# Performance work log

Hardware: AMD Instinct MI355X
Metric: run time of the kernel (lower is better)

## Reference

```python
import jax, jax.numpy as jnp
import numpy as np

N = 262144  # total points
D = 256     # embedding dim
S = 8       # number of subbatches
L = 64      # instance labels per subbatch (label id range)
DELTA_V = 0.5
DELTA_D = 1.5


def setup_inputs() -> dict:
    key = jax.random.key(0)
    k1, k2, k3 = jax.random.split(key, 3)
    outputs = jax.random.normal(k1, (N, D), dtype=jnp.float32)
    labels = jax.random.randint(k2, (N,), 0, L, dtype=jnp.int32)
    subbatch_indices = jax.random.randint(k3, (N,), 0, S, dtype=jnp.int32)
    return {"outputs": outputs, "labels": labels, "subbatch_indices": subbatch_indices}


def reference(outputs, labels, subbatch_indices):
    n = outputs.shape[0]
    # normalize embeddings (L2 norm per point, matching torch.linalg.norm axis=1)
    x = outputs / (jnp.linalg.norm(outputs, axis=1) + 1e-8)[:, None]

    # combined segment id: (subbatch, label) -> subbatch*L + label
    seg = subbatch_indices * L + labels  # [N]
    num_seg = S * L

    ones = jnp.ones((n,), dtype=x.dtype)
    counts = jax.ops.segment_sum(ones, seg, num_segments=num_seg)        # [S*L] Nm per (sb,label)
    sums = jax.ops.segment_sum(x, seg, num_segments=num_seg)             # [S*L, D]
    mus = sums / jnp.maximum(counts, 1.0)[:, None]                        # centroids
    present = counts > 0                                                  # [S*L]
    M = jnp.sum(present.reshape(S, L).astype(x.dtype), axis=1)            # [S] unique labels per subbatch

    # ---- pull term: sum_m sum_{i in m} relu(||mu_m - x_i||_1 - dv)^2 / (M*Nm) ----
    mu_pt = mus[seg]                                                      # [N, D]
    d1 = jnp.sum(jnp.abs(mu_pt - x), axis=1)                              # [N] L1 dist to own centroid
    pull_pt = jax.nn.relu(d1 - DELTA_V) ** 2                              # weights are all 1.0
    denom = M[subbatch_indices] * counts[seg]                             # [N] M_sb * Nm
    L_pull = jax.ops.segment_sum(pull_pt / denom, subbatch_indices, num_segments=S)  # [S]

    # ---- push term: pairwise centroid L1 distances within each subbatch ----
    mus_s = mus.reshape(S, L, D)
    pres = present.reshape(S, L)
    dist = jnp.sum(jnp.abs(mus_s[:, :, None, :] - mus_s[:, None, :, :]), axis=-1)  # [S,L,L]
    pairmask = pres[:, :, None] & pres[:, None, :]
    pairmask = pairmask & (~jnp.eye(L, dtype=bool))[None]
    push = jnp.sum(jnp.where(pairmask, jax.nn.relu(2.0 * DELTA_D - dist) ** 2, 0.0), axis=(1, 2))
    L_push = push / jnp.maximum(M * (M - 1.0), 1.0)                        # [S]

    # only subbatches with M > 1 contribute; divide by B = total number of points
    valid = M > 1.0
    loss = jnp.sum(jnp.where(valid, L_pull + L_push, 0.0)) / n
    return loss
```

## Files before the change

### kernel.cpp

```cpp
#include <hip/hip_runtime.h>

#define DIM 256
#define NSB 8
#define NLBL 64
#define NSEG (NSB * NLBL)
#define NBH 128
#define CAP 576
#define SMEM_BYTES (CAP * 256 + DIM * 4 + 16 * 4)

__global__ void k_hist(const int* __restrict__ labels, const int* __restrict__ sbidx,
                       int* __restrict__ blockBins, int n) {
    __shared__ int bins[NSEG];
    for (int i = threadIdx.x; i < NSEG; i += 256) bins[i] = 0;
    __syncthreads();
    int t4 = blockIdx.x * 256 + threadIdx.x;
    int stride4 = gridDim.x * 256;
    for (int q = t4; q * 4 < n; q += stride4) {
        int4 lb = reinterpret_cast<const int4*>(labels)[q];
        int4 sb = reinterpret_cast<const int4*>(sbidx)[q];
        atomicAdd(&bins[sb.x * NLBL + lb.x], 1);
        atomicAdd(&bins[sb.y * NLBL + lb.y], 1);
        atomicAdd(&bins[sb.z * NLBL + lb.z], 1);
        atomicAdd(&bins[sb.w * NLBL + lb.w], 1);
    }
    __syncthreads();
    for (int i = threadIdx.x; i < NSEG; i += 256)
        blockBins[blockIdx.x * NSEG + i] = bins[i];
}

__global__ void k_scan(const int* __restrict__ blockBins, int* __restrict__ counts,
                       int* __restrict__ offsets, int* __restrict__ cursors,
                       float* __restrict__ Mvals, float* __restrict__ invcnt,
                       float* __restrict__ Lpull, float* __restrict__ pushv,
                       int* __restrict__ ticket) {
    __shared__ int cnt[NSEG];
    int t = threadIdx.x;
    int sum = 0;
    #pragma unroll 4
    for (int b = 0; b < NBH; b++) sum += blockBins[b * NSEG + t];
    cnt[t] = sum;
    counts[t] = sum;
    invcnt[t] = 1.0f / fmaxf((float)sum, 1.0f);
    if (t < NSB) { Lpull[t] = 0.f; pushv[t] = 0.f; }
    if (t == 0) ticket[0] = 0;
    __syncthreads();
    if (t < 64) {
        int lane = t;
        int carry = 0;
        for (int c = 0; c < NSB; c++) {
            int idx = c * 64 + lane;
            int v = cnt[idx];
            int incl = v;
            #pragma unroll
            for (int m = 1; m < 64; m <<= 1) {
                int t2 = __shfl_up(incl, m, 64);
                if (lane >= m) incl += t2;
            }
            int excl = carry + incl - v;
            offsets[idx] = excl;
            cursors[idx] = excl;
            carry += __shfl(incl, 63, 64);
            unsigned long long b = __ballot(v > 0);
            if (lane == 0) Mvals[c] = (float)__popcll(b);
        }
    }
}

__global__ void k_scatter(const int* __restrict__ labels, const int* __restrict__ sbidx,
                          int* __restrict__ cursors, int* __restrict__ sorted, int n) {
    int t = blockIdx.x * blockDim.x + threadIdx.x;
    int stride = gridDim.x * blockDim.x;
    for (int q = t; q * 4 < n; q += stride) {
        int4 lb = reinterpret_cast<const int4*>(labels)[q];
        int4 sb = reinterpret_cast<const int4*>(sbidx)[q];
        int p = q * 4;
        sorted[atomicAdd(&cursors[sb.x * NLBL + lb.x], 1)] = p;
        sorted[atomicAdd(&cursors[sb.y * NLBL + lb.y], 1)] = p + 1;
        sorted[atomicAdd(&cursors[sb.z * NLBL + lb.z], 1)] = p + 2;
        sorted[atomicAdd(&cursors[sb.w * NLBL + lb.w], 1)] = p + 3;
    }
}

__device__ inline unsigned packq(float x, float y, float z, float w, float s) {
    int q0 = (int)rintf(x * s); q0 = max(-127, min(127, q0));
    int q1 = (int)rintf(y * s); q1 = max(-127, min(127, q1));
    int q2 = (int)rintf(z * s); q2 = max(-127, min(127, q2));
    int q3 = (int)rintf(w * s); q3 = max(-127, min(127, q3));
    return (unsigned)(q0 & 255) | ((unsigned)(q1 & 255) << 8) |
           ((unsigned)(q2 & 255) << 16) | ((unsigned)(q3 & 255) << 24);
}

__global__ __launch_bounds__(1024) void k_seg(
    const float* __restrict__ outp, const int* __restrict__ sorted,
    const int* __restrict__ offsets, const int* __restrict__ counts,
    const float* __restrict__ invcnt, float* __restrict__ mus,
    float* __restrict__ Lpull) {
    extern __shared__ unsigned char smem[];
    unsigned* xrows = (unsigned*)smem;
    float* muA  = (float*)(smem + CAP * 256);
    float* wsum = (float*)(smem + CAP * 256 + DIM * 4);

    int seg = blockIdx.x;
    int base = offsets[seg], cnt = counts[seg];
    int tid = threadIdx.x, lane = tid & 63, wv = tid >> 6;
    float ic = invcnt[seg];
    if (tid < DIM) muA[tid] = 0.f;
    __syncthreads();
    if (cnt == 0) {
        if (tid < DIM) mus[(size_t)seg * DIM + tid] = 0.f;
        return;
    }

    float4 acc = {0.f, 0.f, 0.f, 0.f};
    int r = wv * 4;
    int p0 = (r + 0 < cnt) ? sorted[base + r + 0] : -1;
    int p1 = (r + 1 < cnt) ? sorted[base + r + 1] : -1;
    int p2 = (r + 2 < cnt) ? sorted[base + r + 2] : -1;
    int p3 = (r + 3 < cnt) ? sorted[base + r + 3] : -1;
    for (; r < cnt; r += 64) {
        int nr = r + 64;
        int q0 = (nr + 0 < cnt) ? sorted[base + nr + 0] : -1;
        int q1 = (nr + 1 < cnt) ? sorted[base + nr + 1] : -1;
        int q2 = (nr + 2 < cnt) ? sorted[base + nr + 2] : -1;
        int q3 = (nr + 3 < cnt) ? sorted[base + nr + 3] : -1;
        float4 v0 = {0.f,0.f,0.f,0.f}, v1 = {0.f,0.f,0.f,0.f};
        float4 v2 = {0.f,0.f,0.f,0.f}, v3 = {0.f,0.f,0.f,0.f};
        v0 = *reinterpret_cast<const float4*>(outp + (size_t)p0 * DIM + lane * 4);
        if (p1 >= 0) v1 = *reinterpret_cast<const float4*>(outp + (size_t)p1 * DIM + lane * 4);
        if (p2 >= 0) v2 = *reinterpret_cast<const float4*>(outp + (size_t)p2 * DIM + lane * 4);
        if (p3 >= 0) v3 = *reinterpret_cast<const float4*>(outp + (size_t)p3 * DIM + lane * 4);
        float s0 = v0.x*v0.x + v0.y*v0.y + v0.z*v0.z + v0.w*v0.w;
        float s1 = v1.x*v1.x + v1.y*v1.y + v1.z*v1.z + v1.w*v1.w;
        float s2 = v2.x*v2.x + v2.y*v2.y + v2.z*v2.z + v2.w*v2.w;
        float s3 = v3.x*v3.x + v3.y*v3.y + v3.z*v3.z + v3.w*v3.w;
        #pragma unroll
        for (int m = 32; m >= 1; m >>= 1) {
            s0 += __shfl_xor(s0, m, 64);
            s1 += __shfl_xor(s1, m, 64);
            s2 += __shfl_xor(s2, m, 64);
            s3 += __shfl_xor(s3, m, 64);
        }
        float r0 = 1.0f / (sqrtf(s0) + 1e-8f);
        float r1 = 1.0f / (sqrtf(s1) + 1e-8f);
        float r2 = 1.0f / (sqrtf(s2) + 1e-8f);
        float r3 = 1.0f / (sqrtf(s3) + 1e-8f);
        if (r + 0 < CAP)            xrows[(r + 0) * 64 + lane] = packq(v0.x, v0.y, v0.z, v0.w, r0 * 256.f);
        if (p1 >= 0 && r + 1 < CAP) xrows[(r + 1) * 64 + lane] = packq(v1.x, v1.y, v1.z, v1.w, r1 * 256.f);
        if (p2 >= 0 && r + 2 < CAP) xrows[(r + 2) * 64 + lane] = packq(v2.x, v2.y, v2.z, v2.w, r2 * 256.f);
        if (p3 >= 0 && r + 3 < CAP) xrows[(r + 3) * 64 + lane] = packq(v3.x, v3.y, v3.z, v3.w, r3 * 256.f);
        acc.x += v0.x*r0 + v1.x*r1 + v2.x*r2 + v3.x*r3;
        acc.y += v0.y*r0 + v1.y*r1 + v2.y*r2 + v3.y*r3;
        acc.z += v0.z*r0 + v1.z*r1 + v2.z*r2 + v3.z*r3;
        acc.w += v0.w*r0 + v1.w*r1 + v2.w*r2 + v3.w*r3;
        p0 = q0; p1 = q1; p2 = q2; p3 = q3;
    }
    atomicAdd(&muA[lane * 4 + 0], acc.x);
    atomicAdd(&muA[lane * 4 + 1], acc.y);
    atomicAdd(&muA[lane * 4 + 2], acc.z);
    atomicAdd(&muA[lane * 4 + 3], acc.w);
    __syncthreads();
    if (tid < DIM) {
        float mu = muA[tid] * ic;
        muA[tid] = mu;
        mus[(size_t)seg * DIM + tid] = mu;
    }
    __syncthreads();

    float4 mu4 = *reinterpret_cast<const float4*>(muA + lane * 4);
    float4 mu256 = {mu4.x * 256.f, mu4.y * 256.f, mu4.z * 256.f, mu4.w * 256.f};
    float psum = 0.f;
    int m1 = min(cnt, CAP);
    for (int rr = wv * 4; rr < m1; rr += 64) {
        bool b1 = rr + 1 < m1, b2 = rr + 2 < m1, b3 = rr + 3 < m1;
        unsigned w0 = xrows[(rr + 0) * 64 + lane];
        unsigned w1 = b1 ? xrows[(rr + 1) * 64 + lane] : 0u;
        unsigned w2 = b2 ? xrows[(rr + 2) * 64 + lane] : 0u;
        unsigned w3 = b3 ? xrows[(rr + 3) * 64 + lane] : 0u;
        float d0 = fabsf(mu256.x - (float)((int)(w0 << 24) >> 24))
                 + fabsf(mu256.y - (float)((int)(w0 << 16) >> 24))
                 + fabsf(mu256.z - (float)((int)(w0 <<  8) >> 24))
                 + fabsf(mu256.w - (float)((int)w0 >> 24));
        float d1 = fabsf(mu256.x - (float)((int)(w1 << 24) >> 24))
                 + fabsf(mu256.y - (float)((int)(w1 << 16) >> 24))
                 + fabsf(mu256.z - (float)((int)(w1 <<  8) >> 24))
                 + fabsf(mu256.w - (float)((int)w1 >> 24));
        float d2 = fabsf(mu256.x - (float)((int)(w2 << 24) >> 24))
                 + fabsf(mu256.y - (float)((int)(w2 << 16) >> 24))
                 + fabsf(mu256.z - (float)((int)(w2 <<  8) >> 24))
                 + fabsf(mu256.w - (float)((int)w2 >> 24));
        float d3 = fabsf(mu256.x - (float)((int)(w3 << 24) >> 24))
                 + fabsf(mu256.y - (float)((int)(w3 << 16) >> 24))
                 + fabsf(mu256.z - (float)((int)(w3 <<  8) >> 24))
                 + fabsf(mu256.w - (float)((int)w3 >> 24));
        #pragma unroll
        for (int m = 32; m >= 1; m >>= 1) {
            d0 += __shfl_xor(d0, m, 64);
            d1 += __shfl_xor(d1, m, 64);
            d2 += __shfl_xor(d2, m, 64);
            d3 += __shfl_xor(d3, m, 64);
        }
        float t0 = fmaxf(d0 * 0.00390625f - 0.5f, 0.f);
        psum += t0 * t0;
        if (b1) { float t = fmaxf(d1 * 0.00390625f - 0.5f, 0.f); psum += t * t; }
        if (b2) { float t = fmaxf(d2 * 0.00390625f - 0.5f, 0.f); psum += t * t; }
        if (b3) { float t = fmaxf(d3 * 0.00390625f - 0.5f, 0.f); psum += t * t; }
    }
    for (int rr = CAP + wv; rr < cnt; rr += 16) {
        int p = sorted[base + rr];
        float4 v = *reinterpret_cast<const float4*>(outp + (size_t)p * DIM + lane * 4);
        float ss = v.x*v.x + v.y*v.y + v.z*v.z + v.w*v.w;
        #pragma unroll
        for (int m = 32; m >= 1; m >>= 1) ss += __shfl_xor(ss, m, 64);
        float rn = 1.0f / (sqrtf(ss) + 1e-8f);
        float d = fabsf(mu4.x - v.x*rn) + fabsf(mu4.y - v.y*rn)
                + fabsf(mu4.z - v.z*rn) + fabsf(mu4.w - v.w*rn);
        #pragma unroll
        for (int m = 32; m >= 1; m >>= 1) d += __shfl_xor(d, m, 64);
        float t = fmaxf(d - 0.5f, 0.f);
        psum += t * t;
    }
    if (lane == 0) wsum[wv] = psum;
    __syncthreads();
    if (tid == 0) {
        float tot = 0.f;
        #pragma unroll
        for (int w = 0; w < 16; w++) tot += wsum[w];
        atomicAdd(&Lpull[seg >> 6], tot * ic);
    }
}

__global__ void k_final(const float* __restrict__ mus, const int* __restrict__ counts,
                        float* __restrict__ pushv, float* __restrict__ Lpull,
                        const float* __restrict__ Mvals, int* __restrict__ ticket,
                        float* __restrict__ outv, int n) {
    __shared__ float lds[NLBL][DIM + 1];
    __shared__ float wsum[4];
    __shared__ int lastFlag;
    int s = blockIdx.x >> 4;
    int chunk = blockIdx.x & 15;
    for (int i = threadIdx.x; i < NLBL * DIM; i += 256) {
        int r = i >> 8, d = i & 255;
        lds[r][d] = mus[(size_t)(s * NLBL + r) * DIM + d];
    }
    __syncthreads();
    int pair = chunk * 256 + threadIdx.x;
    int l1 = pair >> 6, l2 = pair & 63;
    float dist = 0.0f;
    #pragma unroll 8
    for (int d = 0; d < DIM; d++) dist += fabsf(lds[l1][d] - lds[l2][d]);
    float v = fmaxf(3.0f - dist, 0.0f);
    v = v * v;
    bool ok = (l1 != l2) && (counts[s * NLBL + l1] > 0) && (counts[s * NLBL + l2] > 0);
    v = ok ? v : 0.0f;
    #pragma unroll
    for (int m = 32; m >= 1; m >>= 1) v += __shfl_xor(v, m, 64);
    if ((threadIdx.x & 63) == 0) wsum[threadIdx.x >> 6] = v;
    __syncthreads();
    if (threadIdx.x == 0) {
        atomicAdd(&pushv[s], wsum[0] + wsum[1] + wsum[2] + wsum[3]);
        __threadfence();
        int t = atomicAdd(ticket, 1);
        lastFlag = (t == (int)gridDim.x - 1) ? 1 : 0;
    }
    __syncthreads();
    if (lastFlag && threadIdx.x == 0) {
        float loss = 0.0f;
        for (int q = 0; q < NSB; q++) {
            float M = Mvals[q];
            float pv = atomicAdd(&pushv[q], 0.0f);
            float lpv = atomicAdd(&Lpull[q], 0.0f);
            if (M > 1.0f)
                loss += lpv / M + pv / fmaxf(M * (M - 1.0f), 1.0f);
        }
        outv[0] = loss / (float)n;
    }
}

extern "C" void kernel_launch(void* const* d_in, const int* in_sizes, int n_in,
                              void* d_out, int out_size, void* d_ws, size_t ws_size,
                              hipStream_t stream) {
    const float* outp = (const float*)d_in[0];
    const int* labels = (const int*)d_in[1];
    const int* sbidx = (const int*)d_in[2];
    float* outv = (float*)d_out;
    int n = in_sizes[1];

    float* mus = (float*)d_ws;
    int* sorted = (int*)(mus + (size_t)NSEG * DIM);
    int* blockBins = sorted + n;
    int* counts = blockBins + NBH * NSEG;
    int* offsets = counts + NSEG;
    int* cursors = offsets + NSEG;
    int* ticket = cursors + NSEG;
    float* invcnt = (float*)(ticket + 1);
    float* Mvals = invcnt + NSEG;
    float* Lpull = Mvals + NSB;
    float* pushv = Lpull + NSB;

    hipFuncSetAttribute(reinterpret_cast<const void*>(k_seg),
                        hipFuncAttributeMaxDynamicSharedMemorySize, SMEM_BYTES);

    k_hist<<<NBH, 256, 0, stream>>>(labels, sbidx, blockBins, n);
    k_scan<<<1, 512, 0, stream>>>(blockBins, counts, offsets, cursors, Mvals, invcnt,
                                  Lpull, pushv, ticket);
    k_scatter<<<256, 256, 0, stream>>>(labels, sbidx, cursors, sorted, n);
    k_seg<<<NSEG, 1024, SMEM_BYTES, stream>>>(outp, sorted, offsets, counts, invcnt,
                                              mus, Lpull);
    k_final<<<NSB * 16, 256, 0, stream>>>(mus, counts, pushv, Lpull, Mvals,
                                          ticket, outv, n);
}
```

Before: 190.5 us.

## Pre-normalize and int8-quantize rows in a coalesced pass before segment gather

Adds a k_norm kernel that streams the fp32 embeddings sequentially, L2-normalizes them and packs them to int8 in a workspace buffer. k_seg then gathers these 4x-smaller quantized rows instead of fp32 rows and accumulates the centroids in integer arithmetic. The aim is to replace the random fp32 gather with a coalesced read plus a cheaper gather, and to drop the per-row norm reductions inside k_seg. The cost is an extra kernel launch and a 64 MB write plus reread of the workspace. Centroids now come from quantized values, so accuracy is lower.

Result: slower. 215.9 us (+13.3%).

```diff
diff --git a/kernel.cpp b/kernel.cpp
--- a/kernel.cpp
+++ b/kernel.cpp
@@ -90,13 +90,47 @@
            ((unsigned)(q2 & 255) << 16) | ((unsigned)(q3 & 255) << 24);
 }
 
+__global__ void k_norm(const float* __restrict__ outp, unsigned* __restrict__ xns, int n) {
+    int w = (blockIdx.x * blockDim.x + threadIdx.x) >> 6;
+    int lane = threadIdx.x & 63;
+    int nw = (gridDim.x * blockDim.x) >> 6;
+    for (int pb = w * 4; pb < n; pb += nw * 4) {
+        bool k1 = pb + 1 < n, k2 = pb + 2 < n, k3 = pb + 3 < n;
+        float4 v0 = *reinterpret_cast<const float4*>(outp + (size_t)(pb + 0) * DIM + lane * 4);
+        float4 v1 = {0.f,0.f,0.f,0.f}, v2 = {0.f,0.f,0.f,0.f}, v3 = {0.f,0.f,0.f,0.f};
+        if (k1) v1 = *reinterpret_cast<const float4*>(outp + (size_t)(pb + 1) * DIM + lane * 4);
+        if (k2) v2 = *reinterpret_cast<const float4*>(outp + (size_t)(pb + 2) * DIM + lane * 4);
+        if (k3) v3 = *reinterpret_cast<const float4*>(outp + (size_t)(pb + 3) * DIM + lane * 4);
+        float s0 = v0.x*v0.x + v0.y*v0.y + v0.z*v0.z + v0.w*v0.w;
+        float s1 = v1.x*v1.x + v1.y*v1.y + v1.z*v1.z + v1.w*v1.w;
+        float s2 = v2.x*v2.x + v2.y*v2.y + v2.z*v2.z + v2.w*v2.w;
+        float s3 = v3.x*v3.x + v3.y*v3.y + v3.z*v3.z + v3.w*v3.w;
+        #pragma unroll
+        for (int m = 32; m >= 1; m >>= 1) {
+            s0 += __shfl_xor(s0, m, 64);
+            s1 += __shfl_xor(s1, m, 64);
+            s2 += __shfl_xor(s2, m, 64);
+            s3 += __shfl_xor(s3, m, 64);
+        }
+        float r0 = 256.0f / (sqrtf(s0) + 1e-8f);
+        float r1 = 256.0f / (sqrtf(s1) + 1e-8f);
+        float r2 = 256.0f / (sqrtf(s2) + 1e-8f);
+        float r3 = 256.0f / (sqrtf(s3) + 1e-8f);
+        xns[(size_t)(pb + 0) * 64 + lane] = packq(v0.x, v0.y, v0.z, v0.w, r0);
+        if (k1) xns[(size_t)(pb + 1) * 64 + lane] = packq(v1.x, v1.y, v1.z, v1.w, r1);
+        if (k2) xns[(size_t)(pb + 2) * 64 + lane] = packq(v2.x, v2.y, v2.z, v2.w, r2);
+        if (k3) xns[(size_t)(pb + 3) * 64 + lane] = packq(v3.x, v3.y, v3.z, v3.w, r3);
+    }
+}
+
 __global__ __launch_bounds__(1024) void k_seg(
-    const float* __restrict__ outp, const int* __restrict__ sorted,
+    const unsigned* __restrict__ xns, const int* __restrict__ sorted,
     const int* __restrict__ offsets, const int* __restrict__ counts,
     const float* __restrict__ invcnt, float* __restrict__ mus,
     float* __restrict__ Lpull) {
     extern __shared__ unsigned char smem[];
     unsigned* xrows = (unsigned*)smem;
+    int* muI    = (int*)(smem + CAP * 256);
     float* muA  = (float*)(smem + CAP * 256);
     float* wsum = (float*)(smem + CAP * 256 + DIM * 4);
 
@@ -104,14 +138,14 @@
     int base = offsets[seg], cnt = counts[seg];
     int tid = threadIdx.x, lane = tid & 63, wv = tid >> 6;
     float ic = invcnt[seg];
-    if (tid < DIM) muA[tid] = 0.f;
+    if (tid < DIM) muI[tid] = 0;
     __syncthreads();
     if (cnt == 0) {
         if (tid < DIM) mus[(size_t)seg * DIM + tid] = 0.f;
         return;
     }
 
-    float4 acc = {0.f, 0.f, 0.f, 0.f};
+    int4 acc = {0, 0, 0, 0};
     int r = wv * 4;
     int p0 = (r + 0 < cnt) ? sorted[base + r + 0] : -1;
     int p1 = (r + 1 < cnt) ? sorted[base + r + 1] : -1;
@@ -123,51 +157,37 @@
         int q1 = (nr + 1 < cnt) ? sorted[base + nr + 1] : -1;
         int q2 = (nr + 2 < cnt) ? sorted[base + nr + 2] : -1;
         int q3 = (nr + 3 < cnt) ? sorted[base + nr + 3] : -1;
-        float4 v0 = {0.f,0.f,0.f,0.f}, v1 = {0.f,0.f,0.f,0.f};
-        float4 v2 = {0.f,0.f,0.f,0.f}, v3 = {0.f,0.f,0.f,0.f};
-        v0 = *reinterpret_cast<const float4*>(outp + (size_t)p0 * DIM + lane * 4);
-        if (p1 >= 0) v1 = *reinterpret_cast<const float4*>(outp + (size_t)p1 * DIM + lane * 4);
-        if (p2 >= 0) v2 = *reinterpret_cast<const float4*>(outp + (size_t)p2 * DIM + lane * 4);
-        if (p3 >= 0) v3 = *reinterpret_cast<const float4*>(outp + (size_t)p3 * DIM + lane * 4);
-        float s0 = v0.x*v0.x + v0.y*v0.y + v0.z*v0.z + v0.w*v0.w;
-        float s1 = v1.x*v1.x + v1.y*v1.y + v1.z*v1.z + v1.w*v1.w;
-        float s2 = v2.x*v2.x + v2.y*v2.y + v2.z*v2.z + v2.w*v2.w;
-        float s3 = v3.x*v3.x + v3.y*v3.y + v3.z*v3.z + v3.w*v3.w;
-        #pragma unroll
-        for (int m = 32; m >= 1; m >>= 1) {
-            s0 += __shfl_xor(s0, m, 64);
-            s1 += __shfl_xor(s1, m, 64);
-            s2 += __shfl_xor(s2, m, 64);
-            s3 += __shfl_xor(s3, m, 64);
-        }
-        float r0 = 1.0f / (sqrtf(s0) + 1e-8f);
-        float r1 = 1.0f / (sqrtf(s1) + 1e-8f);
-        float r2 = 1.0f / (sqrtf(s2) + 1e-8f);
-        float r3 = 1.0f / (sqrtf(s3) + 1e-8f);
-        if (r + 0 < CAP)            xrows[(r + 0) * 64 + lane] = packq(v0.x, v0.y, v0.z, v0.w, r0 * 256.f);
-        if (p1 >= 0 && r + 1 < CAP) xrows[(r + 1) * 64 + lane] = packq(v1.x, v1.y, v1.z, v1.w, r1 * 256.f);
-        if (p2 >= 0 && r + 2 < CAP) xrows[(r + 2) * 64 + lane] = packq(v2.x, v2.y, v2.z, v2.w, r2 * 256.f);
-        if (p3 >= 0 && r + 3 < CAP) xrows[(r + 3) * 64 + lane] = packq(v3.x, v3.y, v3.z, v3.w, r3 * 256.f);
-        acc.x += v0.x*r0 + v1.x*r1 + v2.x*r2 + v3.x*r3;
-        acc.y += v0.y*r0 + v1.y*r1 + v2.y*r2 + v3.y*r3;
-        acc.z += v0.z*r0 + v1.z*r1 + v2.z*r2 + v3.z*r3;
-        acc.w += v0.w*r0 + v1.w*r1 + v2.w*r2 + v3.w*r3;
+        unsigned w0 = xns[(size_t)p0 * 64 + lane];
+        unsigned w1 = (p1 >= 0) ? xns[(size_t)p1 * 64 + lane] : 0u;
+        unsigned w2 = (p2 >= 0) ? xns[(size_t)p2 * 64 + lane] : 0u;
+        unsigned w3 = (p3 >= 0) ? xns[(size_t)p3 * 64 + lane] : 0u;
+        if (r + 0 < CAP)            xrows[(r + 0) * 64 + lane] = w0;
+        if (p1 >= 0 && r + 1 < CAP) xrows[(r + 1) * 64 + lane] = w1;
+        if (p2 >= 0 && r + 2 < CAP) xrows[(r + 2) * 64 + lane] = w2;
+        if (p3 >= 0 && r + 3 < CAP) xrows[(r + 3) * 64 + lane] = w3;
+        acc.x += ((int)(w0 << 24) >> 24) + ((int)(w1 << 24) >> 24) +
+                 ((int)(w2 << 24) >> 24) + ((int)(w3 << 24) >> 24);
+        acc.y += ((int)(w0 << 16) >> 24) + ((int)(w1 << 16) >> 24) +
+                 ((int)(w2 << 16) >> 24) + ((int)(w3 << 16) >> 24);
+        acc.z += ((int)(w0 <<  8) >> 24) + ((int)(w1 <<  8) >> 24) +
+                 ((int)(w2 <<  8) >> 24) + ((int)(w3 <<  8) >> 24);
+        acc.w += ((int)w0 >> 24) + ((int)w1 >> 24) +
+                 ((int)w2 >> 24) + ((int)w3 >> 24);
         p0 = q0; p1 = q1; p2 = q2; p3 = q3;
     }
-    atomicAdd(&muA[lane * 4 + 0], acc.x);
-    atomicAdd(&muA[lane * 4 + 1], acc.y);
-    atomicAdd(&muA[lane * 4 + 2], acc.z);
-    atomicAdd(&muA[lane * 4 + 3], acc.w);
+    atomicAdd(&muI[lane * 4 + 0], acc.x);
+    atomicAdd(&muI[lane * 4 + 1], acc.y);
+    atomicAdd(&muI[lane * 4 + 2], acc.z);
+    atomicAdd(&muI[lane * 4 + 3], acc.w);
     __syncthreads();
     if (tid < DIM) {
-        float mu = muA[tid] * ic;
-        muA[tid] = mu;
-        mus[(size_t)seg * DIM + tid] = mu;
-    }
-    __syncthreads();
-
-    float4 mu4 = *reinterpret_cast<const float4*>(muA + lane * 4);
-    float4 mu256 = {mu4.x * 256.f, mu4.y * 256.f, mu4.z * 256.f, mu4.w * 256.f};
+        float t = (float)muI[tid];
+        mus[(size_t)seg * DIM + tid] = t * ic * 0.00390625f;
+        muA[tid] = t * ic;
+    }
+    __syncthreads();
+
+    float4 mu256 = *reinterpret_cast<const float4*>(muA + lane * 4);
     float psum = 0.f;
     int m1 = min(cnt, CAP);
     for (int rr = wv * 4; rr < m1; rr += 64) {
@@ -207,16 +227,14 @@
     }
     for (int rr = CAP + wv; rr < cnt; rr += 16) {
         int p = sorted[base + rr];
-        float4 v = *reinterpret_cast<const float4*>(outp + (size_t)p * DIM + lane * 4);
-        float ss = v.x*v.x + v.y*v.y + v.z*v.z + v.w*v.w;
-        #pragma unroll
-        for (int m = 32; m >= 1; m >>= 1) ss += __shfl_xor(ss, m, 64);
-        float rn = 1.0f / (sqrtf(ss) + 1e-8f);
-        float d = fabsf(mu4.x - v.x*rn) + fabsf(mu4.y - v.y*rn)
-                + fabsf(mu4.z - v.z*rn) + fabsf(mu4.w - v.w*rn);
+        unsigned w0 = xns[(size_t)p * 64 + lane];
+        float d = fabsf(mu256.x - (float)((int)(w0 << 24) >> 24))
+                + fabsf(mu256.y - (float)((int)(w0 << 16) >> 24))
+                + fabsf(mu256.z - (float)((int)(w0 <<  8) >> 24))
+                + fabsf(mu256.w - (float)((int)w0 >> 24));
         #pragma unroll
         for (int m = 32; m >= 1; m >>= 1) d += __shfl_xor(d, m, 64);
-        float t = fmaxf(d - 0.5f, 0.f);
+        float t = fmaxf(d * 0.00390625f - 0.5f, 0.f);
         psum += t * t;
     }
     if (lane == 0) wsum[wv] = psum;
@@ -285,7 +303,8 @@
     float* outv = (float*)d_out;
     int n = in_sizes[1];
 
-    float* mus = (float*)d_ws;
+    unsigned* xns = (unsigned*)d_ws;
+    float* mus = (float*)(xns + (size_t)n * 64);
     int* sorted = (int*)(mus + (size_t)NSEG * DIM);
     int* blockBins = sorted + n;
     int* counts = blockBins + NBH * NSEG;
@@ -304,7 +323,8 @@
     k_scan<<<1, 512, 0, stream>>>(blockBins, counts, offsets, cursors, Mvals, invcnt,
                                   Lpull, pushv, ticket);
     k_scatter<<<256, 256, 0, stream>>>(labels, sbidx, cursors, sorted, n);
-    k_seg<<<NSEG, 1024, SMEM_BYTES, stream>>>(outp, sorted, offsets, counts, invcnt,
+    k_norm<<<2048, 256, 0, stream>>>(outp, xns, n);
+    k_seg<<<NSEG, 1024, SMEM_BYTES, stream>>>(xns, sorted, offsets, counts, invcnt,
                                               mus, Lpull);
     k_final<<<NSB * 16, 256, 0, stream>>>(mus, counts, pushv, Lpull, Mvals,
                                           ticket, outv, n);
```

## Spill quantized rows to global scratch instead of LDS, pad segments to 64

Applied to the files above, without the earlier changes.

The int8-quantized normalized rows move out of a large per-block LDS buffer into a global scratch array. This removes the 144KB dynamic shared memory so more blocks can be resident per CU. Segment offsets are padded to multiples of 64 so rows can be read as int4 index loads and processed branch-free with 0/1 weights. The slow full-precision overflow path for segments larger than the LDS capacity is gone. The cost is extra global write and read traffic for the quantized rows, which should mostly hit L2/MALL, plus padded-row indices that depend on uninitialized sorted entries being clamped.

Measured after the change: 209.9 us. 10.2% more time.

```diff
diff --git a/kernel.cpp b/kernel.cpp
--- a/kernel.cpp
+++ b/kernel.cpp
@@ -5,8 +5,6 @@
 #define NLBL 64
 #define NSEG (NSB * NLBL)
 #define NBH 128
-#define CAP 576
-#define SMEM_BYTES (CAP * 256 + DIM * 4 + 16 * 4)
 
 __global__ void k_hist(const int* __restrict__ labels, const int* __restrict__ sbidx,
                        int* __restrict__ blockBins, int n) {
@@ -36,7 +34,7 @@
     __shared__ int cnt[NSEG];
     int t = threadIdx.x;
     int sum = 0;
-    #pragma unroll 4
+    #pragma unroll 8
     for (int b = 0; b < NBH; b++) sum += blockBins[b * NSEG + t];
     cnt[t] = sum;
     counts[t] = sum;
@@ -50,13 +48,14 @@
         for (int c = 0; c < NSB; c++) {
             int idx = c * 64 + lane;
             int v = cnt[idx];
-            int incl = v;
+            int vr = (v + 63) & ~63;
+            int incl = vr;
             #pragma unroll
             for (int m = 1; m < 64; m <<= 1) {
                 int t2 = __shfl_up(incl, m, 64);
                 if (lane >= m) incl += t2;
             }
-            int excl = carry + incl - v;
+            int excl = carry + incl - vr;
             offsets[idx] = excl;
             cursors[idx] = excl;
             carry += __shfl(incl, 63, 64);
@@ -90,45 +89,37 @@
            ((unsigned)(q2 & 255) << 16) | ((unsigned)(q3 & 255) << 24);
 }
 
-__global__ __launch_bounds__(1024) void k_seg(
+__global__ __launch_bounds__(1024, 8) void k_seg(
     const float* __restrict__ outp, const int* __restrict__ sorted,
     const int* __restrict__ offsets, const int* __restrict__ counts,
-    const float* __restrict__ invcnt, float* __restrict__ mus,
-    float* __restrict__ Lpull) {
-    extern __shared__ unsigned char smem[];
-    unsigned* xrows = (unsigned*)smem;
-    float* muA  = (float*)(smem + CAP * 256);
-    float* wsum = (float*)(smem + CAP * 256 + DIM * 4);
-
+    const float* __restrict__ invcnt, unsigned* __restrict__ xq,
+    float* __restrict__ mus, float* __restrict__ Lpull, int n) {
+    __shared__ float muA[DIM];
+    __shared__ float wsum[16];
     int seg = blockIdx.x;
     int base = offsets[seg], cnt = counts[seg];
+    int cntR = (cnt + 63) & ~63;
     int tid = threadIdx.x, lane = tid & 63, wv = tid >> 6;
     float ic = invcnt[seg];
+    unsigned pmax = (unsigned)(n - 1);
     if (tid < DIM) muA[tid] = 0.f;
     __syncthreads();
-    if (cnt == 0) {
-        if (tid < DIM) mus[(size_t)seg * DIM + tid] = 0.f;
-        return;
-    }
-
-    float4 acc = {0.f, 0.f, 0.f, 0.f};
-    int r = wv * 4;
-    int p0 = (r + 0 < cnt) ? sorted[base + r + 0] : -1;
-    int p1 = (r + 1 < cnt) ? sorted[base + r + 1] : -1;
-    int p2 = (r + 2 < cnt) ? sorted[base + r + 2] : -1;
-    int p3 = (r + 3 < cnt) ? sorted[base + r + 3] : -1;
-    for (; r < cnt; r += 64) {
-        int nr = r + 64;
-        int q0 = (nr + 0 < cnt) ? sorted[base + nr + 0] : -1;
-        int q1 = (nr + 1 < cnt) ? sorted[base + nr + 1] : -1;
-        int q2 = (nr + 2 < cnt) ? sorted[base + nr + 2] : -1;
-        int q3 = (nr + 3 < cnt) ? sorted[base + nr + 3] : -1;
-        float4 v0 = {0.f,0.f,0.f,0.f}, v1 = {0.f,0.f,0.f,0.f};
-        float4 v2 = {0.f,0.f,0.f,0.f}, v3 = {0.f,0.f,0.f,0.f};
-        v0 = *reinterpret_cast<const float4*>(outp + (size_t)p0 * DIM + lane * 4);
-        if (p1 >= 0) v1 = *reinterpret_cast<const float4*>(outp + (size_t)p1 * DIM + lane * 4);
-        if (p2 >= 0) v2 = *reinterpret_cast<const float4*>(outp + (size_t)p2 * DIM + lane * 4);
-        if (p3 >= 0) v3 = *reinterpret_cast<const float4*>(outp + (size_t)p3 * DIM + lane * 4);
+
+    float ax = 0.f, ay = 0.f, az = 0.f, aw = 0.f;
+    for (int r = wv * 4; r < cntR; r += 64) {
+        int4 id4 = *reinterpret_cast<const int4*>(sorted + base + r);
+        unsigned p0 = min((unsigned)id4.x, pmax);
+        unsigned p1 = min((unsigned)id4.y, pmax);
+        unsigned p2 = min((unsigned)id4.z, pmax);
+        unsigned p3 = min((unsigned)id4.w, pmax);
+        float w0 = (r + 0 < cnt) ? 1.f : 0.f;
+        float w1 = (r + 1 < cnt) ? 1.f : 0.f;
+        float w2 = (r + 2 < cnt) ? 1.f : 0.f;
+        float w3 = (r + 3 < cnt) ? 1.f : 0.f;
+        float4 v0 = *reinterpret_cast<const float4*>(outp + (size_t)p0 * DIM + lane * 4);
+        float4 v1 = *reinterpret_cast<const float4*>(outp + (size_t)p1 * DIM + lane * 4);
+        float4 v2 = *reinterpret_cast<const float4*>(outp + (size_t)p2 * DIM + lane * 4);
+        float4 v3 = *reinterpret_cast<const float4*>(outp + (size_t)p3 * DIM + lane * 4);
         float s0 = v0.x*v0.x + v0.y*v0.y + v0.z*v0.z + v0.w*v0.w;
         float s1 = v1.x*v1.x + v1.y*v1.y + v1.z*v1.z + v1.w*v1.w;
         float s2 = v2.x*v2.x + v2.y*v2.y + v2.z*v2.z + v2.w*v2.w;
@@ -140,42 +131,39 @@
             s2 += __shfl_xor(s2, m, 64);
             s3 += __shfl_xor(s3, m, 64);
         }
-        float r0 = 1.0f / (sqrtf(s0) + 1e-8f);
-        float r1 = 1.0f / (sqrtf(s1) + 1e-8f);
-        float r2 = 1.0f / (sqrtf(s2) + 1e-8f);
-        float r3 = 1.0f / (sqrtf(s3) + 1e-8f);
-        if (r + 0 < CAP)            xrows[(r + 0) * 64 + lane] = packq(v0.x, v0.y, v0.z, v0.w, r0 * 256.f);
-        if (p1 >= 0 && r + 1 < CAP) xrows[(r + 1) * 64 + lane] = packq(v1.x, v1.y, v1.z, v1.w, r1 * 256.f);
-        if (p2 >= 0 && r + 2 < CAP) xrows[(r + 2) * 64 + lane] = packq(v2.x, v2.y, v2.z, v2.w, r2 * 256.f);
-        if (p3 >= 0 && r + 3 < CAP) xrows[(r + 3) * 64 + lane] = packq(v3.x, v3.y, v3.z, v3.w, r3 * 256.f);
-        acc.x += v0.x*r0 + v1.x*r1 + v2.x*r2 + v3.x*r3;
-        acc.y += v0.y*r0 + v1.y*r1 + v2.y*r2 + v3.y*r3;
-        acc.z += v0.z*r0 + v1.z*r1 + v2.z*r2 + v3.z*r3;
-        acc.w += v0.w*r0 + v1.w*r1 + v2.w*r2 + v3.w*r3;
-        p0 = q0; p1 = q1; p2 = q2; p3 = q3;
-    }
-    atomicAdd(&muA[lane * 4 + 0], acc.x);
-    atomicAdd(&muA[lane * 4 + 1], acc.y);
-    atomicAdd(&muA[lane * 4 + 2], acc.z);
-    atomicAdd(&muA[lane * 4 + 3], acc.w);
+        float r0 = 256.0f / (sqrtf(s0) + 1e-8f);
+        float r1 = 256.0f / (sqrtf(s1) + 1e-8f);
+        float r2 = 256.0f / (sqrtf(s2) + 1e-8f);
+        float r3 = 256.0f / (sqrtf(s3) + 1e-8f);
+        xq[(size_t)(base + r + 0) * 64 + lane] = packq(v0.x, v0.y, v0.z, v0.w, r0);
+        xq[(size_t)(base + r + 1) * 64 + lane] = packq(v1.x, v1.y, v1.z, v1.w, r1);
+        xq[(size_t)(base + r + 2) * 64 + lane] = packq(v2.x, v2.y, v2.z, v2.w, r2);
+        xq[(size_t)(base + r + 3) * 64 + lane] = packq(v3.x, v3.y, v3.z, v3.w, r3);
+        float f0 = r0 * w0, f1 = r1 * w1, f2 = r2 * w2, f3 = r3 * w3;
+        ax += v0.x*f0 + v1.x*f1 + v2.x*f2 + v3.x*f3;
+        ay += v0.y*f0 + v1.y*f1 + v2.y*f2 + v3.y*f3;
+        az += v0.z*f0 + v1.z*f1 + v2.z*f2 + v3.z*f3;
+        aw += v0.w*f0 + v1.w*f1 + v2.w*f2 + v3.w*f3;
+    }
+    atomicAdd(&muA[lane * 4 + 0], ax);
+    atomicAdd(&muA[lane * 4 + 1], ay);
+    atomicAdd(&muA[lane * 4 + 2], az);
+    atomicAdd(&muA[lane * 4 + 3], aw);
     __syncthreads();
     if (tid < DIM) {
-        float mu = muA[tid] * ic;
-        muA[tid] = mu;
-        mus[(size_t)seg * DIM + tid] = mu;
-    }
-    __syncthreads();
-
-    float4 mu4 = *reinterpret_cast<const float4*>(muA + lane * 4);
-    float4 mu256 = {mu4.x * 256.f, mu4.y * 256.f, mu4.z * 256.f, mu4.w * 256.f};
+        float s = muA[tid] * ic;
+        mus[(size_t)seg * DIM + tid] = s * 0.00390625f;
+        muA[tid] = s;
+    }
+    __syncthreads();
+
+    float4 mu256 = *reinterpret_cast<const float4*>(muA + lane * 4);
     float psum = 0.f;
-    int m1 = min(cnt, CAP);
-    for (int rr = wv * 4; rr < m1; rr += 64) {
-        bool b1 = rr + 1 < m1, b2 = rr + 2 < m1, b3 = rr + 3 < m1;
-        unsigned w0 = xrows[(rr + 0) * 64 + lane];
-        unsigned w1 = b1 ? xrows[(rr + 1) * 64 + lane] : 0u;
-        unsigned w2 = b2 ? xrows[(rr + 2) * 64 + lane] : 0u;
-        unsigned w3 = b3 ? xrows[(rr + 3) * 64 + lane] : 0u;
+    for (int r = wv * 4; r < cntR; r += 64) {
+        unsigned w0 = xq[(size_t)(base + r + 0) * 64 + lane];
+        unsigned w1 = xq[(size_t)(base + r + 1) * 64 + lane];
+        unsigned w2 = xq[(size_t)(base + r + 2) * 64 + lane];
+        unsigned w3 = xq[(size_t)(base + r + 3) * 64 + lane];
         float d0 = fabsf(mu256.x - (float)((int)(w0 << 24) >> 24))
                  + fabsf(mu256.y - (float)((int)(w0 << 16) >> 24))
                  + fabsf(mu256.z - (float)((int)(w0 <<  8) >> 24))
@@ -199,25 +187,15 @@
             d2 += __shfl_xor(d2, m, 64);
             d3 += __shfl_xor(d3, m, 64);
         }
+        float u0 = (r + 0 < cnt) ? 1.f : 0.f;
+        float u1 = (r + 1 < cnt) ? 1.f : 0.f;
+        float u2 = (r + 2 < cnt) ? 1.f : 0.f;
+        float u3 = (r + 3 < cnt) ? 1.f : 0.f;
         float t0 = fmaxf(d0 * 0.00390625f - 0.5f, 0.f);
-        psum += t0 * t0;
-        if (b1) { float t = fmaxf(d1 * 0.00390625f - 0.5f, 0.f); psum += t * t; }
-        if (b2) { float t = fmaxf(d2 * 0.00390625f - 0.5f, 0.f); psum += t * t; }
-        if (b3) { float t = fmaxf(d3 * 0.00390625f - 0.5f, 0.f); psum += t * t; }
-    }
-    for (int rr = CAP + wv; rr < cnt; rr += 16) {
-        int p = sorted[base + rr];
-        float4 v = *reinterpret_cast<const float4*>(outp + (size_t)p * DIM + lane * 4);
-        float ss = v.x*v.x + v.y*v.y + v.z*v.z + v.w*v.w;
-        #pragma unroll
-        for (int m = 32; m >= 1; m >>= 1) ss += __shfl_xor(ss, m, 64);
-        float rn = 1.0f / (sqrtf(ss) + 1e-8f);
-        float d = fabsf(mu4.x - v.x*rn) + fabsf(mu4.y - v.y*rn)
-                + fabsf(mu4.z - v.z*rn) + fabsf(mu4.w - v.w*rn);
-        #pragma unroll
-        for (int m = 32; m >= 1; m >>= 1) d += __shfl_xor(d, m, 64);
-        float t = fmaxf(d - 0.5f, 0.f);
-        psum += t * t;
+        float t1 = fmaxf(d1 * 0.00390625f - 0.5f, 0.f);
+        float t2 = fmaxf(d2 * 0.00390625f - 0.5f, 0.f);
+        float t3 = fmaxf(d3 * 0.00390625f - 0.5f, 0.f);
+        psum += u0*t0*t0 + u1*t1*t1 + u2*t2*t2 + u3*t3*t3;
     }
     if (lane == 0) wsum[wv] = psum;
     __syncthreads();
@@ -285,9 +263,12 @@
     float* outv = (float*)d_out;
     int n = in_sizes[1];
 
-    float* mus = (float*)d_ws;
+    int capTotal = n + NSEG * 64;
+
+    unsigned* xq = (unsigned*)d_ws;
+    float* mus = (float*)(xq + (size_t)capTotal * 64);
     int* sorted = (int*)(mus + (size_t)NSEG * DIM);
-    int* blockBins = sorted + n;
+    int* blockBins = sorted + capTotal;
     int* counts = blockBins + NBH * NSEG;
     int* offsets = counts + NSEG;
     int* cursors = offsets + NSEG;
@@ -297,15 +278,12 @@
     float* Lpull = Mvals + NSB;
     float* pushv = Lpull + NSB;
 
-    hipFuncSetAttribute(reinterpret_cast<const void*>(k_seg),
-                        hipFuncAttributeMaxDynamicSharedMemorySize, SMEM_BYTES);
-
     k_hist<<<NBH, 256, 0, stream>>>(labels, sbidx, blockBins, n);
     k_scan<<<1, 512, 0, stream>>>(blockBins, counts, offsets, cursors, Mvals, invcnt,
                                   Lpull, pushv, ticket);
     k_scatter<<<256, 256, 0, stream>>>(labels, sbidx, cursors, sorted, n);
-    k_seg<<<NSEG, 1024, SMEM_BYTES, stream>>>(outp, sorted, offsets, counts, invcnt,
-                                              mus, Lpull);
+    k_seg<<<NSEG, 1024, 0, stream>>>(outp, sorted, offsets, counts, invcnt,
+                                     xq, mus, Lpull, n);
     k_final<<<NSB * 16, 256, 0, stream>>>(mus, counts, pushv, Lpull, Mvals,
                                           ticket, outv, n);
 }
```

## Split each segment across two blocks with global atomic centroid reduction and spin-wait

Applied to the files above, without the earlier changes.

Each (subbatch,label) segment is now handled by two 512-thread blocks instead of one 1024-thread block. Each block stores half the rows in its LDS cache, adds a partial centroid sum into a global buffer with atomics, and then spin-waits on a per-segment counter until both halves finish before computing pull distances. The intent is to halve the LDS footprint per block so more blocks fit per CU and occupancy improves. The cost is an extra zeroing kernel, global atomics, and an inter-block spin-wait that can deadlock if the two partner blocks are not co-resident. The scatter grid is also doubled and the scan unroll raised.

Result: slower. 210.6 us (+10.5%).

```diff
diff --git a/kernel.cpp b/kernel.cpp
--- a/kernel.cpp
+++ b/kernel.cpp
@@ -5,8 +5,9 @@
 #define NLBL 64
 #define NSEG (NSB * NLBL)
 #define NBH 128
-#define CAP 576
-#define SMEM_BYTES (CAP * 256 + DIM * 4 + 16 * 4)
+#define BPS 2
+#define CAP 288
+#define SMEM_BYTES (CAP * 256 + DIM * 4 + 8 * 4)
 
 __global__ void k_hist(const int* __restrict__ labels, const int* __restrict__ sbidx,
                        int* __restrict__ blockBins, int n) {
@@ -36,7 +37,7 @@
     __shared__ int cnt[NSEG];
     int t = threadIdx.x;
     int sum = 0;
-    #pragma unroll 4
+    #pragma unroll 8
     for (int b = 0; b < NBH; b++) sum += blockBins[b * NSEG + t];
     cnt[t] = sum;
     counts[t] = sum;
@@ -90,39 +91,46 @@
            ((unsigned)(q2 & 255) << 16) | ((unsigned)(q3 & 255) << 24);
 }
 
-__global__ __launch_bounds__(1024) void k_seg(
+__global__ __launch_bounds__(512) void k_seg(
     const float* __restrict__ outp, const int* __restrict__ sorted,
     const int* __restrict__ offsets, const int* __restrict__ counts,
-    const float* __restrict__ invcnt, float* __restrict__ mus,
+    const float* __restrict__ invcnt, float* __restrict__ mu_sums,
+    int* __restrict__ segdone, float* __restrict__ mus,
     float* __restrict__ Lpull) {
     extern __shared__ unsigned char smem[];
     unsigned* xrows = (unsigned*)smem;
     float* muA  = (float*)(smem + CAP * 256);
     float* wsum = (float*)(smem + CAP * 256 + DIM * 4);
-
-    int seg = blockIdx.x;
+    __shared__ int segLast;
+
+    int seg = blockIdx.x >> 1;
+    int part = blockIdx.x & 1;
     int base = offsets[seg], cnt = counts[seg];
     int tid = threadIdx.x, lane = tid & 63, wv = tid >> 6;
     float ic = invcnt[seg];
     if (tid < DIM) muA[tid] = 0.f;
     __syncthreads();
     if (cnt == 0) {
-        if (tid < DIM) mus[(size_t)seg * DIM + tid] = 0.f;
+        if (part == 0 && tid < DIM) mus[(size_t)seg * DIM + tid] = 0.f;
         return;
     }
+    int half = (cnt + 1) >> 1;
+    int lo = part * half;
+    int hi = min(cnt, lo + half);
+    int myN = hi - lo;
 
     float4 acc = {0.f, 0.f, 0.f, 0.f};
     int r = wv * 4;
-    int p0 = (r + 0 < cnt) ? sorted[base + r + 0] : -1;
-    int p1 = (r + 1 < cnt) ? sorted[base + r + 1] : -1;
-    int p2 = (r + 2 < cnt) ? sorted[base + r + 2] : -1;
-    int p3 = (r + 3 < cnt) ? sorted[base + r + 3] : -1;
-    for (; r < cnt; r += 64) {
-        int nr = r + 64;
-        int q0 = (nr + 0 < cnt) ? sorted[base + nr + 0] : -1;
-        int q1 = (nr + 1 < cnt) ? sorted[base + nr + 1] : -1;
-        int q2 = (nr + 2 < cnt) ? sorted[base + nr + 2] : -1;
-        int q3 = (nr + 3 < cnt) ? sorted[base + nr + 3] : -1;
+    int p0 = (r + 0 < myN) ? sorted[base + lo + r + 0] : -1;
+    int p1 = (r + 1 < myN) ? sorted[base + lo + r + 1] : -1;
+    int p2 = (r + 2 < myN) ? sorted[base + lo + r + 2] : -1;
+    int p3 = (r + 3 < myN) ? sorted[base + lo + r + 3] : -1;
+    for (; r < myN; r += 32) {
+        int nr = r + 32;
+        int q0 = (nr + 0 < myN) ? sorted[base + lo + nr + 0] : -1;
+        int q1 = (nr + 1 < myN) ? sorted[base + lo + nr + 1] : -1;
+        int q2 = (nr + 2 < myN) ? sorted[base + lo + nr + 2] : -1;
+        int q3 = (nr + 3 < myN) ? sorted[base + lo + nr + 3] : -1;
         float4 v0 = {0.f,0.f,0.f,0.f}, v1 = {0.f,0.f,0.f,0.f};
         float4 v2 = {0.f,0.f,0.f,0.f}, v3 = {0.f,0.f,0.f,0.f};
         v0 = *reinterpret_cast<const float4*>(outp + (size_t)p0 * DIM + lane * 4);
@@ -159,18 +167,29 @@
     atomicAdd(&muA[lane * 4 + 2], acc.z);
     atomicAdd(&muA[lane * 4 + 3], acc.w);
     __syncthreads();
-    if (tid < DIM) {
-        float mu = muA[tid] * ic;
-        muA[tid] = mu;
-        mus[(size_t)seg * DIM + tid] = mu;
-    }
-    __syncthreads();
-
-    float4 mu4 = *reinterpret_cast<const float4*>(muA + lane * 4);
-    float4 mu256 = {mu4.x * 256.f, mu4.y * 256.f, mu4.z * 256.f, mu4.w * 256.f};
+    if (tid < DIM) atomicAdd(&mu_sums[(size_t)seg * DIM + tid], muA[tid]);
+    __syncthreads();
+    if (tid == 0) {
+        __threadfence();
+        segLast = (atomicAdd(&segdone[seg], 1) == BPS - 1) ? 1 : 0;
+    }
+    __syncthreads();
+    if (segLast && tid < DIM)
+        mus[(size_t)seg * DIM + tid] = atomicAdd(&mu_sums[(size_t)seg * DIM + tid], 0.f) * ic;
+    __syncthreads();
+    if (tid == 0) {
+        while (atomicAdd(&segdone[seg], 0) < BPS) { __builtin_amdgcn_s_sleep(8); }
+        segLast = 1;
+    }
+    __syncthreads();
+    if (tid < DIM)
+        muA[tid] = atomicAdd(&mu_sums[(size_t)seg * DIM + tid], 0.f) * ic * 256.f;
+    __syncthreads();
+
+    float4 mu256 = *reinterpret_cast<const float4*>(muA + lane * 4);
     float psum = 0.f;
-    int m1 = min(cnt, CAP);
-    for (int rr = wv * 4; rr < m1; rr += 64) {
+    int m1 = min(myN, CAP);
+    for (int rr = wv * 4; rr < m1; rr += 32) {
         bool b1 = rr + 1 < m1, b2 = rr + 2 < m1, b3 = rr + 3 < m1;
         unsigned w0 = xrows[(rr + 0) * 64 + lane];
         unsigned w1 = b1 ? xrows[(rr + 1) * 64 + lane] : 0u;
@@ -205,15 +224,15 @@
         if (b2) { float t = fmaxf(d2 * 0.00390625f - 0.5f, 0.f); psum += t * t; }
         if (b3) { float t = fmaxf(d3 * 0.00390625f - 0.5f, 0.f); psum += t * t; }
     }
-    for (int rr = CAP + wv; rr < cnt; rr += 16) {
-        int p = sorted[base + rr];
+    for (int rr = CAP + wv; rr < myN; rr += 8) {
+        int p = sorted[base + lo + rr];
         float4 v = *reinterpret_cast<const float4*>(outp + (size_t)p * DIM + lane * 4);
         float ss = v.x*v.x + v.y*v.y + v.z*v.z + v.w*v.w;
         #pragma unroll
         for (int m = 32; m >= 1; m >>= 1) ss += __shfl_xor(ss, m, 64);
         float rn = 1.0f / (sqrtf(ss) + 1e-8f);
-        float d = fabsf(mu4.x - v.x*rn) + fabsf(mu4.y - v.y*rn)
-                + fabsf(mu4.z - v.z*rn) + fabsf(mu4.w - v.w*rn);
+        float d = fabsf(mu256.x * 0.00390625f - v.x*rn) + fabsf(mu256.y * 0.00390625f - v.y*rn)
+                + fabsf(mu256.z * 0.00390625f - v.z*rn) + fabsf(mu256.w * 0.00390625f - v.w*rn);
         #pragma unroll
         for (int m = 32; m >= 1; m >>= 1) d += __shfl_xor(d, m, 64);
         float t = fmaxf(d - 0.5f, 0.f);
@@ -224,7 +243,7 @@
     if (tid == 0) {
         float tot = 0.f;
         #pragma unroll
-        for (int w = 0; w < 16; w++) tot += wsum[w];
+        for (int w = 0; w < 8; w++) tot += wsum[w];
         atomicAdd(&Lpull[seg >> 6], tot * ic);
     }
 }
@@ -276,6 +295,12 @@
     }
 }
 
+__global__ void k_zero(float* __restrict__ mu_sums, int* __restrict__ segdone) {
+    int t = blockIdx.x * 256 + threadIdx.x;
+    if (t < NSEG * DIM) mu_sums[t] = 0.f;
+    if (t < NSEG) segdone[t] = 0;
+}
+
 extern "C" void kernel_launch(void* const* d_in, const int* in_sizes, int n_in,
                               void* d_out, int out_size, void* d_ws, size_t ws_size,
                               hipStream_t stream) {
@@ -286,7 +311,9 @@
     int n = in_sizes[1];
 
     float* mus = (float*)d_ws;
-    int* sorted = (int*)(mus + (size_t)NSEG * DIM);
+    float* mu_sums = mus + (size_t)NSEG * DIM;
+    int* segdone = (int*)(mu_sums + (size_t)NSEG * DIM);
+    int* sorted = segdone + NSEG;
     int* blockBins = sorted + n;
     int* counts = blockBins + NBH * NSEG;
     int* offsets = counts + NSEG;
@@ -300,12 +327,13 @@
     hipFuncSetAttribute(reinterpret_cast<const void*>(k_seg),
                         hipFuncAttributeMaxDynamicSharedMemorySize, SMEM_BYTES);
 
+    k_zero<<<(NSEG * DIM + 255) / 256, 256, 0, stream>>>(mu_sums, segdone);
     k_hist<<<NBH, 256, 0, stream>>>(labels, sbidx, blockBins, n);
     k_scan<<<1, 512, 0, stream>>>(blockBins, counts, offsets, cursors, Mvals, invcnt,
                                   Lpull, pushv, ticket);
-    k_scatter<<<256, 256, 0, stream>>>(labels, sbidx, cursors, sorted, n);
-    k_seg<<<NSEG, 1024, SMEM_BYTES, stream>>>(outp, sorted, offsets, counts, invcnt,
-                                              mus, Lpull);
+    k_scatter<<<512, 256, 0, stream>>>(labels, sbidx, cursors, sorted, n);
+    k_seg<<<NSEG * BPS, 512, SMEM_BYTES, stream>>>(outp, sorted, offsets, counts, invcnt,
+                                                   mu_sums, segdone, mus, Lpull);
     k_final<<<NSB * 16, 256, 0, stream>>>(mus, counts, pushv, Lpull, Mvals,
                                           ticket, outv, n);
 }
```
